# Kernel optimization log

Hardware: AMD Instinct MI355X
Metric: run time of the kernel (lower is better)

## Reference

```python
import jax, jax.numpy as jnp
import numpy as np

V_TH = 1.0  # IF neuron threshold (default v_threshold=1, v_reset=0)
SCALE = 1.0  # PoissonEncoder firing scale


def setup_inputs() -> dict:
    key = jax.random.key(0)
    k_x, k_n, k_w1, k_w2 = jax.random.split(key, 4)
    B, T, D_IN, D_H, D_OUT = 8192, 32, 784, 100, 10
    x = jax.random.uniform(k_x, (B, D_IN), dtype=jnp.float32)
    noise = jax.random.uniform(k_n, (T, B, D_IN), dtype=jnp.float32)
    W1 = jax.random.normal(k_w1, (D_H, D_IN), dtype=jnp.float32) * (1.0 / np.sqrt(D_IN))
    W2 = jax.random.normal(k_w2, (D_OUT, D_H), dtype=jnp.float32) * (1.0 / np.sqrt(D_H))
    return {"x": x, "noise": noise, "W1": W1, "W2": W2}


def reference(x, noise, W1, W2):
    # Poisson encoding: spike if uniform noise < scale * firing_rate.  [T,B,784]
    spikes = jnp.where(noise < SCALE * x[None, :, :], 1.0, 0.0).astype(x.dtype)

    B = x.shape[0]
    v0 = jnp.zeros((B, W1.shape[0]), dtype=x.dtype)          # membrane potential [B,100]
    logits0 = jnp.zeros((B, W2.shape[0]), dtype=x.dtype)      # accumulated logits [B,10]

    def step(carry, sp_t):
        v, logits = carry
        h = jnp.einsum('bi,hi->bh', sp_t, W1)                 # Linear 784->100 (no bias)
        v = v + h                                             # integrate
        spike = jnp.where(v - V_TH > 0, 1.0, 0.0).astype(h.dtype)  # fire
        v = v - spike * V_TH                                  # soft reset
        logits = logits + jnp.einsum('bh,oh->bo', spike, W2)  # Linear 100->10, accumulate
        return (v, logits), None

    (_, logits), _ = jax.lax.scan(step, (v0, logits0), spikes)
    return logits
```

## Files before the change

kernel.cpp:

```cpp
#include <hip/hip_runtime.h>
#include <hip/hip_bf16.h>
#include <cstdint>


typedef __attribute__((ext_vector_type(8))) short bf16x8;
typedef __attribute__((ext_vector_type(4))) float f32x4;

#define D_IN 784
#define NB 8192
#define KT 25
#define NTL 8
#define DH 100

__global__ void prep_w1(const float* __restrict__ W1, unsigned short* __restrict__ wf) {
    int idx = blockIdx.x * 256 + threadIdx.x;
    if (idx >= KT * NTL * 64) return;
    int l  = idx & 63;
    int nt = (idx >> 6) & 7;
    int kt = idx >> 9;
    int n  = nt * 16 + (l & 15);
    int i0 = kt * 32 + (l >> 4) * 8;
    size_t fbase = (size_t)(kt * 8 + nt) * 1024;
    #pragma unroll
    for (int j = 0; j < 8; ++j) {
        int i = i0 + j;
        float w = (n < DH && i < D_IN) ? W1[n * D_IN + i] : 0.f;
        uint32_t ub = __float_as_uint(w);
        uint32_t rh = ub + 0x7FFFu + ((ub >> 16) & 1u);
        unsigned short h = (unsigned short)(rh >> 16);
        float hf = __uint_as_float(((uint32_t)h) << 16);
        float resid = w - hf;
        uint32_t ul = __float_as_uint(resid);
        uint32_t rl = ul + 0x7FFFu + ((ul >> 16) & 1u);
        unsigned short lo = (unsigned short)(rl >> 16);
        wf[fbase + l * 8 + j]       = h;
        wf[fbase + 512 + l * 8 + j] = lo;
    }
}

__global__ __launch_bounds__(256) void spike_pack(const float* __restrict__ x,
                                                  const float* __restrict__ noise,
                                                  uint32_t* __restrict__ bits) {
    const int tid  = threadIdx.x;
    const int lane = tid & 63;
    const int w    = blockIdx.x * 4 + (tid >> 6);
    const int kt   = w % 25;
    const int bp   = w / 25;
    const int b    = bp * 2 + (lane >> 5);
    const int i    = kt * 32 + (lane & 31);
    const int ic   = i < D_IN ? i : D_IN - 1;
    const bool valid = (i < D_IN);
    const size_t ro = (size_t)b * D_IN + ic;
    const float xv  = x[ro];
    float nv[32];
    #pragma unroll
    for (int t = 0; t < 32; ++t)
        nv[t] = noise[(size_t)t * ((size_t)NB * D_IN) + ro];
    #pragma unroll
    for (int t = 0; t < 32; ++t) {
        unsigned long long m = __ballot(valid && (nv[t] < xv));
        if ((lane & 31) == 0)
            bits[(size_t)(t * KT + kt) * NB + b] = (uint32_t)(m >> lane);
    }
}

__global__ __launch_bounds__(256) void bit_gemm(const uint32_t* __restrict__ bits,
                                                const unsigned short* __restrict__ wf,
                                                float* __restrict__ H) {
    const int tid   = threadIdx.x;
    const int lane  = tid & 63;
    const int wave  = tid >> 6;
    const int Mhalf = wave >> 1;
    const int Nhalf = wave & 1;
    const int bid   = blockIdx.x;
    const int btile = bid & 63;
    const int t     = bid >> 6;
    const int b0    = btile * 128;
    const int rowBase = b0 + Mhalf * 64 + (lane & 15);
    const int sh      = (lane >> 4) * 8;

    f32x4 acc[4][4];
    #pragma unroll
    for (int i = 0; i < 4; ++i)
        #pragma unroll
        for (int j = 0; j < 4; ++j) acc[i][j] = (f32x4){0.f, 0.f, 0.f, 0.f};

    #pragma unroll 2
    for (int kt = 0; kt < KT; ++kt) {
        const uint32_t* bptr = bits + (size_t)(t * KT + kt) * NB;
        uint32_t g[4];
        #pragma unroll
        for (int mt = 0; mt < 4; ++mt) g[mt] = bptr[rowBase + mt * 16];

        bf16x8 afr[4];
        #pragma unroll
        for (int mt = 0; mt < 4; ++mt) {
            union { uint32_t u[4]; bf16x8 v; } pk;
            #pragma unroll
            for (int d = 0; d < 4; ++d) {
                const uint32_t b2 = (g[mt] >> (sh + d * 2)) & 3u;
                pk.u[d] = ((b2 & 1u) ? 0x3F80u : 0u) | ((b2 & 2u) ? 0x3F800000u : 0u);
            }
            afr[mt] = pk.v;
        }
        #pragma unroll
        for (int nt = 0; nt < 4; ++nt) {
            const size_t fo = (size_t)(kt * 8 + Nhalf * 4 + nt) * 1024 + lane * 8;
            const bf16x8 bhi = *reinterpret_cast<const bf16x8*>(wf + fo);
            const bf16x8 blo = *reinterpret_cast<const bf16x8*>(wf + fo + 512);
            #pragma unroll
            for (int mt = 0; mt < 4; ++mt) {
                acc[mt][nt] = __builtin_amdgcn_mfma_f32_16x16x32_bf16(afr[mt], bhi, acc[mt][nt], 0, 0, 0);
                acc[mt][nt] = __builtin_amdgcn_mfma_f32_16x16x32_bf16(afr[mt], blo, acc[mt][nt], 0, 0, 0);
            }
        }
    }
    const int colBase   = Nhalf * 64 + (lane & 15);
    const int rowInTile = (lane >> 4) * 4;
    #pragma unroll
    for (int mt = 0; mt < 4; ++mt) {
        const size_t rg = (size_t)t * NB + b0 + Mhalf * 64 + mt * 16 + rowInTile;
        #pragma unroll
        for (int nt = 0; nt < 4; ++nt) {
            const int col = colBase + nt * 16;
            if (col < DH) {
                #pragma unroll
                for (int r = 0; r < 4; ++r)
                    H[(rg + r) * DH + col] = acc[mt][nt][r];
            }
        }
    }
}

__global__ __launch_bounds__(256) void snn_scan(const float* __restrict__ H,
                                                const float* __restrict__ W2,
                                                float* __restrict__ out) {
    __shared__ float cbuf[2][104];
    __shared__ float w2s[1000];
    const int tid = threadIdx.x;
    const int r = tid >> 7, h = tid & 127;
    const size_t b = (size_t)blockIdx.x * 2 + r;
    for (int i = tid; i < 1000; i += 256) w2s[i] = W2[i];

    float cnt = 0.f;
    if (h < DH) {
        float hv[32];
        #pragma unroll
        for (int t = 0; t < 32; ++t) hv[t] = H[((size_t)t * NB + b) * DH + h];
        float v = 0.f;
        #pragma unroll
        for (int t = 0; t < 32; ++t) {
            v += hv[t];
            float s = (v - 1.0f > 0.0f) ? 1.0f : 0.0f;
            v -= s;
            cnt += s;
        }
    }
    if (h < DH) cbuf[r][h] = cnt;
    __syncthreads();
    if (tid < 20) {
        const int rr = tid / 10, o = tid % 10;
        float s = 0.f;
        for (int hh = 0; hh < DH; ++hh) s += cbuf[rr][hh] * w2s[o * DH + hh];
        out[((size_t)blockIdx.x * 2 + rr) * 10 + o] = s;
    }
}

extern "C" void kernel_launch(void* const* d_in, const int* in_sizes, int n_in,
                              void* d_out, int out_size, void* d_ws, size_t ws_size,
                              hipStream_t stream) {
    const float* x     = (const float*)d_in[0];
    const float* noise = (const float*)d_in[1];
    const float* W1    = (const float*)d_in[2];
    const float* W2    = (const float*)d_in[3];
    float* out = (float*)d_out;

    unsigned short* wf = (unsigned short*)d_ws;
    uint32_t* bits = (uint32_t*)((char*)d_ws + (1u << 20));
    float* H = (float*)((char*)d_ws + (32u << 20));

    prep_w1<<<50, 256, 0, stream>>>(W1, wf);
    spike_pack<<<25600, 256, 0, stream>>>(x, noise, bits);
    bit_gemm<<<2048, 256, 0, stream>>>(bits, wf, H);
    snn_scan<<<4096, 256, 0, stream>>>(H, W2, out);
}
```

Before: 370.0 us.

## Stream noise contiguously per batch tile with LDS bit transpose; make H batch-major

```diff
diff --git a/kernel.cpp b/kernel.cpp
--- a/kernel.cpp
+++ b/kernel.cpp
@@ -38,29 +38,58 @@
     }
 }
 
-__global__ __launch_bounds__(256) void spike_pack(const float* __restrict__ x,
-                                                  const float* __restrict__ noise,
-                                                  uint32_t* __restrict__ bits) {
+__global__ __launch_bounds__(256) void pack_contig(const float* __restrict__ x,
+                                                   const float* __restrict__ noise,
+                                                   uint32_t* __restrict__ bits) {
+    __shared__ __align__(4) unsigned short sB[128 * 50];
     const int tid  = threadIdx.x;
     const int lane = tid & 63;
-    const int w    = blockIdx.x * 4 + (tid >> 6);
-    const int kt   = w % 25;
-    const int bp   = w / 25;
-    const int b    = bp * 2 + (lane >> 5);
-    const int i    = kt * 32 + (lane & 31);
-    const int ic   = i < D_IN ? i : D_IN - 1;
-    const bool valid = (i < D_IN);
-    const size_t ro = (size_t)b * D_IN + ic;
-    const float xv  = x[ro];
-    float nv[32];
-    #pragma unroll
-    for (int t = 0; t < 32; ++t)
-        nv[t] = noise[(size_t)t * ((size_t)NB * D_IN) + ro];
-    #pragma unroll
-    for (int t = 0; t < 32; ++t) {
-        unsigned long long m = __ballot(valid && (nv[t] < xv));
-        if ((lane & 31) == 0)
-            bits[(size_t)(t * KT + kt) * NB + b] = (uint32_t)(m >> lane);
+    const int wave = tid >> 6;
+    const int L     = blockIdx.x;
+    const int btile = (L & 7) * 8 + ((L >> 3) & 7);
+    const int t     = L >> 6;
+    const int b0    = btile * 128;
+    const float* nb = noise + (size_t)t * ((size_t)NB * D_IN) + (size_t)b0 * D_IN;
+    const float* xb = x + (size_t)b0 * D_IN;
+
+    if (tid < 128) sB[tid * 50 + 49] = 0;
+
+    const int u = lane & 15;
+    float4 nA, xA;
+    nA = *reinterpret_cast<const float4*>(nb + (size_t)tid * 4);
+    xA = *reinterpret_cast<const float4*>(xb + (size_t)tid * 4);
+    #pragma unroll 2
+    for (int p = 0; p < 98; ++p) {
+        const float4 nC = nA, xC = xA;
+        if (p < 97) {
+            const size_t fo = (size_t)(p + 1) * 256 + tid;
+            nA = *reinterpret_cast<const float4*>(nb + fo * 4);
+            xA = *reinterpret_cast<const float4*>(xb + fo * 4);
+        }
+        const unsigned long long m0 = __ballot(nC.x < xC.x);
+        const unsigned long long m1 = __ballot(nC.y < xC.y);
+        const unsigned long long m2 = __ballot(nC.z < xC.z);
+        const unsigned long long m3 = __ballot(nC.w < xC.w);
+        if (lane < 16) {
+            const uint32_t v = (uint32_t)((m0 >> (4 * u)) & 15ull)
+                             | ((uint32_t)((m1 >> (4 * u)) & 15ull) << 4)
+                             | ((uint32_t)((m2 >> (4 * u)) & 15ull) << 8)
+                             | ((uint32_t)((m3 >> (4 * u)) & 15ull) << 12);
+            const int g = p * 64 + wave * 16 + u;
+            const uint32_t row = ((uint32_t)g * 42800u) >> 21;
+            const int colu = g - (int)row * 49;
+            sB[row * 50 + colu] = (unsigned short)v;
+        }
+    }
+    __syncthreads();
+    const uint32_t* s32 = reinterpret_cast<const uint32_t*>(sB);
+    #pragma unroll
+    for (int p = 0; p < 13; ++p) {
+        const int idx = p * 256 + tid;
+        if (idx < 3200) {
+            const int kt = idx >> 7, bl = idx & 127;
+            bits[(size_t)(t * KT + kt) * NB + b0 + bl] = s32[bl * 25 + kt];
+        }
     }
 }
 
@@ -77,7 +106,8 @@
     const int t     = bid >> 6;
     const int b0    = btile * 128;
     const int rowBase = b0 + Mhalf * 64 + (lane & 15);
-    const int sh      = (lane >> 4) * 8;
+    const int lg      = lane >> 4;
+    const int qe0     = (lg & 1) * 2 + (lg >> 1) * 16;
 
     f32x4 acc[4][4];
     #pragma unroll
@@ -98,8 +128,9 @@
             union { uint32_t u[4]; bf16x8 v; } pk;
             #pragma unroll
             for (int d = 0; d < 4; ++d) {
-                const uint32_t b2 = (g[mt] >> (sh + d * 2)) & 3u;
-                pk.u[d] = ((b2 & 1u) ? 0x3F80u : 0u) | ((b2 & 2u) ? 0x3F800000u : 0u);
+                const int qe = qe0 + (d & 1) * 8 + (d >> 1);
+                pk.u[d] = ((g[mt] >> qe) & 1u) * 0x3F80u
+                        | ((g[mt] >> (qe + 4)) & 1u) * 0x3F800000u;
             }
             afr[mt] = pk.v;
         }
@@ -119,14 +150,14 @@
     const int rowInTile = (lane >> 4) * 4;
     #pragma unroll
     for (int mt = 0; mt < 4; ++mt) {
-        const size_t rg = (size_t)t * NB + b0 + Mhalf * 64 + mt * 16 + rowInTile;
+        const int rowG = b0 + Mhalf * 64 + mt * 16 + rowInTile;
         #pragma unroll
         for (int nt = 0; nt < 4; ++nt) {
             const int col = colBase + nt * 16;
             if (col < DH) {
                 #pragma unroll
                 for (int r = 0; r < 4; ++r)
-                    H[(rg + r) * DH + col] = acc[mt][nt][r];
+                    H[(size_t)(rowG + r) * (32 * DH) + t * DH + col] = acc[mt][nt][r];
             }
         }
     }
@@ -146,7 +177,7 @@
     if (h < DH) {
         float hv[32];
         #pragma unroll
-        for (int t = 0; t < 32; ++t) hv[t] = H[((size_t)t * NB + b) * DH + h];
+        for (int t = 0; t < 32; ++t) hv[t] = H[b * (32 * DH) + t * DH + h];
         float v = 0.f;
         #pragma unroll
         for (int t = 0; t < 32; ++t) {
@@ -180,7 +211,7 @@
     float* H = (float*)((char*)d_ws + (32u << 20));
 
     prep_w1<<<50, 256, 0, stream>>>(W1, wf);
-    spike_pack<<<25600, 256, 0, stream>>>(x, noise, bits);
+    pack_contig<<<2048, 256, 0, stream>>>(x, noise, bits);
     bit_gemm<<<2048, 256, 0, stream>>>(bits, wf, H);
     snn_scan<<<4096, 256, 0, stream>>>(H, W2, out);
 }
```

Measured after the change: 364.2 us. Within noise of the previous version (-1.6%).
